# Kernel tuning notes

Hardware: AMD Instinct MI355X
Metric: run time of the kernel (lower is better)

## Reference

```python
import jax, jax.numpy as jnp
import numpy as np

ROUTING_ITERS = 3


def _squash(x, axis=-1):
    # sum_sq/(1+sum_sq) * x/sqrt(sum_sq), faithful to the torch squash
    sum_sq = jnp.sum(x * x, axis=axis, keepdims=True)
    return sum_sq / (1.0 + sum_sq) * x / jnp.sqrt(sum_sq)


def setup_inputs() -> dict:
    key = jax.random.key(0)
    k1, k2 = jax.random.split(key)
    B, I, O, Din, Dout = 256, 1152, 10, 8, 16
    x = jax.random.normal(k1, (B, I, Din), dtype=jnp.float32)
    W = jax.random.normal(k2, (I, O, Din, Dout), dtype=jnp.float32)
    return {"x": x, "W": W}


def reference(x, W):
    # x: [B, I, Din], W: [I, O, Din, Dout]
    I, O, Din, Dout = W.shape
    # u_hat = x @ W per (capsule_in, capsule_out): [B, I, O, Dout]
    u_hat = jnp.einsum('bid,iode->bioe', x, W)
    b = jnp.zeros((I, O), dtype=x.dtype)  # coupling logits, shared over batch
    v = None
    for _ in range(ROUTING_ITERS):
        c = jax.nn.softmax(b, axis=1)                    # softmax over out capsules
        s = jnp.einsum('bioe,io->boe', u_hat, c)         # weighted sum over in caps
        v = _squash(s, axis=-1)                          # [B, O, Dout]
        # agreement, averaged over batch (torch does .mean(dim=0))
        agree = jnp.einsum('bioe,boe->bio', u_hat, v).mean(axis=0)  # [I, O]
        b = b + agree
    # torch returns v.squeeze(1).transpose(2,3) -> [B, O, Dout, 1]
    return v[..., None]
```

## Files before the change

kernel.cpp:

```cpp
#include <hip/hip_runtime.h>
#include <math.h>

#define B    256
#define I    1152
#define O    10
#define DIN  8
#define DOUT 16
#define OE   160
#define XROW 9216
#define WROW 1280
#define PSPLIT 72
#define CHUNK  16
#define SI     8
#define GRID   288

#define WPREP_JOBS 720

typedef __attribute__((ext_vector_type(8))) short short8;
typedef __attribute__((ext_vector_type(4))) float floatx4;

#define AL(p)    __hip_atomic_load((p),      __ATOMIC_RELAXED, __HIP_MEMORY_SCOPE_AGENT)
#define AS(p, v) __hip_atomic_store((p), (v), __ATOMIC_RELAXED, __HIP_MEMORY_SCOPE_AGENT)

__device__ __forceinline__ unsigned short f2bf(float f) {
    unsigned u = __builtin_bit_cast(unsigned, f);
    u += 0x7fffu + ((u >> 16) & 1u);
    return (unsigned short)(u >> 16);
}
__device__ __forceinline__ float bf2f(unsigned short h) {
    unsigned u = ((unsigned)h) << 16;
    return __builtin_bit_cast(float, u);
}

__device__ __forceinline__ void gbar_full(unsigned* cnt, unsigned* gen)
{
    __syncthreads();
    if (threadIdx.x == 0) {
        __builtin_amdgcn_fence(__ATOMIC_RELEASE, "agent");
        unsigned g = __hip_atomic_load(gen, __ATOMIC_RELAXED, __HIP_MEMORY_SCOPE_AGENT);
        unsigned a = __hip_atomic_fetch_add(cnt, 1u, __ATOMIC_RELAXED, __HIP_MEMORY_SCOPE_AGENT);
        if (a == GRID - 1u) {
            __hip_atomic_store(cnt, 0u, __ATOMIC_RELAXED, __HIP_MEMORY_SCOPE_AGENT);
            __hip_atomic_store(gen, g + 1u, __ATOMIC_RELAXED, __HIP_MEMORY_SCOPE_AGENT);
        } else {
            unsigned spins = 0;
            while (__hip_atomic_load(gen, __ATOMIC_RELAXED, __HIP_MEMORY_SCOPE_AGENT) == g) {
                __builtin_amdgcn_s_sleep(4);
                if (++spins > (1u << 20)) break;
            }
        }
        __builtin_amdgcn_fence(__ATOMIC_ACQUIRE, "agent");
    }
    __syncthreads();
}

__device__ __forceinline__ void gbar_light(unsigned* cnt, unsigned* gen)
{
    __syncthreads();
    if (threadIdx.x == 0) {
        unsigned g = __hip_atomic_load(gen, __ATOMIC_RELAXED, __HIP_MEMORY_SCOPE_AGENT);
        unsigned a = __hip_atomic_fetch_add(cnt, 1u, __ATOMIC_RELAXED, __HIP_MEMORY_SCOPE_AGENT);
        if (a == GRID - 1u) {
            __hip_atomic_store(cnt, 0u, __ATOMIC_RELAXED, __HIP_MEMORY_SCOPE_AGENT);
            __hip_atomic_store(gen, g + 1u, __ATOMIC_RELEASE, __HIP_MEMORY_SCOPE_AGENT);
        } else {
            unsigned spins = 0;
            while (__hip_atomic_load(gen, __ATOMIC_RELAXED, __HIP_MEMORY_SCOPE_AGENT) == g) {
                __builtin_amdgcn_s_sleep(4);
                if (++spins > (1u << 20)) break;
            }
        }
    }
    __syncthreads();
}

__device__ __forceinline__ void stage_prep(
    int bid, int t,
    const float* __restrict__ x, const float* __restrict__ W,
    float* __restrict__ Wt,
    unsigned short* __restrict__ xTh, unsigned short* __restrict__ xTl,
    unsigned short* __restrict__ xh,  unsigned short* __restrict__ xl)
{
#pragma unroll
    for (int r = 0; r < 3; ++r) {
        int job = bid + GRID * r;
        if (job < WPREP_JOBS) {
            int g  = job * 256 + t;
            int i  = g / OE;
            int oe = g - i * OE;
            int o  = oe >> 4;
            int e  = oe & 15;
            const float* wp = W + (size_t)i * WROW + o * (DIN * DOUT) + e;
            float4 a, b;
            a.x = wp[0 * DOUT]; a.y = wp[1 * DOUT]; a.z = wp[2 * DOUT]; a.w = wp[3 * DOUT];
            b.x = wp[4 * DOUT]; b.y = wp[5 * DOUT]; b.z = wp[6 * DOUT]; b.w = wp[7 * DOUT];
            float4* dst = (float4*)(Wt + (size_t)g * 8);
            dst[0] = a;
            dst[1] = b;
        }
    }
#pragma unroll
    for (int r = 0; r < 4; ++r) {
        int g2  = bid + GRID * r;
        int idb = g2 % 144;
        int bb  = g2 / 144;
        int id  = idb * 64 + (t & 63);
        int b0  = bb * 32 + (t >> 6) * 8;
        float v[8];
#pragma unroll
        for (int j = 0; j < 8; ++j)
            v[j] = x[(size_t)(b0 + j) * XROW + id];
        short8 h8, l8;
#pragma unroll
        for (int j = 0; j < 8; ++j) {
            unsigned short h = f2bf(v[j]);
            h8[j] = (short)h;
            l8[j] = (short)f2bf(v[j] - bf2f(h));
        }
        *(short8*)(xTh + (size_t)id * B + b0) = h8;
        *(short8*)(xTl + (size_t)id * B + b0) = l8;
    }
#pragma unroll
    for (int r = 0; r < 8; ++r) {
        int g = (bid + GRID * r) * 256 + t;
        float4 v = ((const float4*)x)[g];
        ushort4 h, l;
        h.x = f2bf(v.x); l.x = f2bf(v.x - bf2f(h.x));
        h.y = f2bf(v.y); l.y = f2bf(v.y - bf2f(h.y));
        h.z = f2bf(v.z); l.z = f2bf(v.z - bf2f(h.z));
        h.w = f2bf(v.w); l.w = f2bf(v.w - bf2f(h.w));
        ((ushort4*)xh)[g] = h;
        ((ushort4*)xl)[g] = l;
    }
}

__device__ __forceinline__ void stage_spart(
    int bid, int t,
    unsigned short* __restrict__ Wh, unsigned short* __restrict__ Wl,
    float (*brow_s)[10], float (*cL)[10],
    const unsigned short* __restrict__ xh, const unsigned short* __restrict__ xl,
    const float* __restrict__ Wt,
    const float* __restrict__ a0, const float* __restrict__ a1,
    float* __restrict__ sp, int it)
{
    int ic  = bid >> 2;
    int mb  = (bid >> 1) & 1;
    int nb  = bid & 1;
    int b0  = mb * 128;
    int oe0 = nb * 80;
    int i0  = ic * CHUNK;

    int w    = t >> 6;
    int lane = t & 63;
    int l15  = lane & 15;
    int q    = lane >> 4;

    if (it) {
        if (t < 160) {
            int iL = t / 10;
            int o  = t - iL * 10;
            int i  = i0 + iL;
            float bo = AL(&a0[i * O + o]) * (1.f / (float)B);
            if (it == 2) bo += AL(&a1[i * O + o]) * (1.f / (float)B);
            brow_s[iL][o] = bo;
        }
        __syncthreads();
        if (t < 16) {
            float m = brow_s[t][0];
#pragma unroll
            for (int o = 1; o < O; ++o) m = fmaxf(m, brow_s[t][o]);
            float ex[O];
            float sum = 0.f;
#pragma unroll
            for (int o = 0; o < O; ++o) { ex[o] = __expf(brow_s[t][o] - m); sum += ex[o]; }
            float inv = 1.f / sum;
#pragma unroll
            for (int o = 0; o < O; ++o) cL[t][o] = ex[o] * inv;
        }
        __syncthreads();
    }

    floatx4 acc[2][5];
#pragma unroll
    for (int mt = 0; mt < 2; ++mt)
#pragma unroll
        for (int nt = 0; nt < 5; ++nt) acc[mt][nt] = (floatx4)(0.f);

#pragma unroll
    for (int round = 0; round < CHUNK / SI; ++round) {
        int si0 = i0 + round * SI;
        if (round) __syncthreads();

        short8 ah[2][2], al[2][2];
#pragma unroll
        for (int ks = 0; ks < 2; ++ks)
#pragma unroll
            for (int mt = 0; mt < 2; ++mt) {
                size_t goff = (size_t)(b0 + w * 32 + mt * 16 + l15) * XROW
                            + (size_t)si0 * 8 + (ks << 5) + (q << 3);
                ah[ks][mt] = *(const short8*)(xh + goff);
                al[ks][mt] = *(const short8*)(xl + goff);
            }

#pragma unroll
        for (int r = 0; r < 3; ++r) {
            int p = t + 256 * r;
            if (p < 640) {
                int oeL = p % 80;
                int iL  = p / 80;
                int o   = (oe0 + oeL) >> 4;
                const float* wp = Wt + ((size_t)(si0 + iL) * OE + oe0 + oeL) * 8;
                float cv = it ? cL[round * SI + iL][o] : 0.1f;
                float4 w0 = *(const float4*)wp;
                float4 w1 = *(const float4*)(wp + 4);
                float wv[8] = {w0.x, w0.y, w0.z, w0.w, w1.x, w1.y, w1.z, w1.w};
                short8 hv, lv;
#pragma unroll
                for (int d = 0; d < 8; ++d) {
                    float s = wv[d] * cv;
                    unsigned short h = f2bf(s);
                    hv[d] = (short)h;
                    lv[d] = (short)f2bf(s - bf2f(h));
                }
                int off = oeL * 64 + ((iL ^ (oeL & 7)) << 3);
                *(short8*)(Wh + off) = hv;
                *(short8*)(Wl + off) = lv;
            }
        }
        __syncthreads();

#pragma unroll
        for (int ks = 0; ks < 2; ++ks) {
#pragma unroll
            for (int nt = 0; nt < 5; ++nt) {
                int rn  = nt * 16 + l15;
                int off = rn * 64 + ((((ks << 2) + q) ^ (rn & 7)) << 3);
                short8 bh = *(const short8*)(Wh + off);
                short8 bl = *(const short8*)(Wl + off);
#pragma unroll
                for (int mt = 0; mt < 2; ++mt) {
                    acc[mt][nt] = __builtin_amdgcn_mfma_f32_16x16x32_bf16(ah[ks][mt], bh, acc[mt][nt], 0, 0, 0);
                    acc[mt][nt] = __builtin_amdgcn_mfma_f32_16x16x32_bf16(ah[ks][mt], bl, acc[mt][nt], 0, 0, 0);
                    acc[mt][nt] = __builtin_amdgcn_mfma_f32_16x16x32_bf16(al[ks][mt], bh, acc[mt][nt], 0, 0, 0);
                }
            }
        }
    }

    float* base = sp + (size_t)ic * (B * OE);
#pragma unroll
    for (int mt = 0; mt < 2; ++mt) {
        int row0 = b0 + w * 32 + mt * 16 + q * 4;
#pragma unroll
        for (int nt = 0; nt < 5; ++nt) {
            int col = oe0 + nt * 16 + l15;
#pragma unroll
            for (int reg = 0; reg < 4; ++reg)
                AS(&base[(row0 + reg) * OE + col], acc[mt][nt][reg]);
        }
    }
}

__device__ __forceinline__ void stage_vred(
    int bid, int t, const float* __restrict__ sp, float* __restrict__ out,
    unsigned* __restrict__ vT, int last)
{
    if (bid >= 160) return;
    int g = bid * 256 + t;
    float s = 0.f;
#pragma unroll 8
    for (int ic = 0; ic < PSPLIT; ++ic) s += AL(&sp[(size_t)ic * (B * OE) + g]);

    float ss = s * s;
    ss += __shfl_xor(ss, 1, 16);
    ss += __shfl_xor(ss, 2, 16);
    ss += __shfl_xor(ss, 4, 16);
    ss += __shfl_xor(ss, 8, 16);
    float f = sqrtf(ss) / (1.f + ss);
    float val = s * f;

    if (last) {
        out[g] = val;
    } else {
        int b  = g / OE;
        int oe = g - b * OE;
        unsigned short h = f2bf(val);
        unsigned pack = (unsigned)h | ((unsigned)f2bf(val - bf2f(h)) << 16);
        AS(&vT[oe * B + b], pack);
    }
}

__device__ __forceinline__ void stage_ggemm(
    int bid, int t,
    unsigned short* __restrict__ Vh, unsigned short* __restrict__ Vl,
    const unsigned short* __restrict__ xTh, const unsigned short* __restrict__ xTl,
    const unsigned* __restrict__ vT,
    const float* __restrict__ Wt, float* __restrict__ agree)
{
    if (bid >= 144) return;
    int m0  = (bid >> 1) * 128;
    int nb  = bid & 1;
    int oe0 = nb * 80;

    int w    = t >> 6;
    int lane = t & 63;
    int l15  = lane & 15;
    int q    = lane >> 4;

    floatx4 acc[2][5];
#pragma unroll
    for (int mt = 0; mt < 2; ++mt)
#pragma unroll
        for (int nt = 0; nt < 5; ++nt) acc[mt][nt] = (floatx4)(0.f);

#pragma unroll
    for (int win = 0; win < 4; ++win) {
        int k0 = win * 64;
        if (win) __syncthreads();

#pragma unroll
        for (int r = 0; r < 3; ++r) {
            int p = t + 256 * r;
            if (p < 640) {
                int row = p >> 3;
                int ch  = p & 7;
                const unsigned long long* vp =
                    (const unsigned long long*)(vT + (size_t)(oe0 + row) * B + k0 + (ch << 3));
                short8 hv, lv;
#pragma unroll
                for (int j = 0; j < 4; ++j) {
                    unsigned long long u = AL(&vp[j]);
                    unsigned lo = (unsigned)u, hi = (unsigned)(u >> 32);
                    hv[2 * j]     = (short)(lo & 0xffffu);
                    lv[2 * j]     = (short)(lo >> 16);
                    hv[2 * j + 1] = (short)(hi & 0xffffu);
                    lv[2 * j + 1] = (short)(hi >> 16);
                }
                int off = row * 64 + ((ch ^ (row & 7)) << 3);
                *(short8*)(Vh + off) = hv;
                *(short8*)(Vl + off) = lv;
            }
        }
        __syncthreads();

        short8 ah[2][2], al[2][2];
#pragma unroll
        for (int ks = 0; ks < 2; ++ks)
#pragma unroll
            for (int mt = 0; mt < 2; ++mt) {
                size_t ga = (size_t)(m0 + w * 32 + mt * 16 + l15) * B
                          + k0 + (ks << 5) + (q << 3);
                ah[ks][mt] = *(const short8*)(xTh + ga);
                al[ks][mt] = *(const short8*)(xTl + ga);
            }

#pragma unroll
        for (int ks = 0; ks < 2; ++ks) {
#pragma unroll
            for (int nt = 0; nt < 5; ++nt) {
                int rn  = nt * 16 + l15;
                int off = rn * 64 + ((((ks << 2) + q) ^ (rn & 7)) << 3);
                short8 bh = *(const short8*)(Vh + off);
                short8 bl = *(const short8*)(Vl + off);
#pragma unroll
                for (int mt = 0; mt < 2; ++mt) {
                    acc[mt][nt] = __builtin_amdgcn_mfma_f32_16x16x32_bf16(ah[ks][mt], bh, acc[mt][nt], 0, 0, 0);
                    acc[mt][nt] = __builtin_amdgcn_mfma_f32_16x16x32_bf16(ah[ks][mt], bl, acc[mt][nt], 0, 0, 0);
                    acc[mt][nt] = __builtin_amdgcn_mfma_f32_16x16x32_bf16(al[ks][mt], bh, acc[mt][nt], 0, 0, 0);
                }
            }
        }
    }

#pragma unroll
    for (int mt = 0; mt < 2; ++mt) {
        int rb = m0 + w * 32 + mt * 16 + q * 4;
        int i  = rb >> 3;
        int d0 = rb & 7;
#pragma unroll
        for (int nt = 0; nt < 5; ++nt) {
            int oe = oe0 + nt * 16 + l15;
            float4 wv = *(const float4*)(Wt + (size_t)i * WROW + oe * 8 + d0);
            floatx4 a = acc[mt][nt];
            float p = a[0] * wv.x + a[1] * wv.y + a[2] * wv.z + a[3] * wv.w;
            p += __shfl_xor(p, 1);
            p += __shfl_xor(p, 2);
            p += __shfl_xor(p, 4);
            p += __shfl_xor(p, 8);
            p += __shfl_xor(p, 16);
            if ((lane & 31) == 0)
                AS(&agree[i * O + nb * 5 + nt], p);
        }
    }
}

__global__ __launch_bounds__(256, 2) void mega_kernel(
    const float* __restrict__ x, const float* __restrict__ W,
    float* __restrict__ out, float* __restrict__ Wt,
    unsigned short* __restrict__ xTh, unsigned short* __restrict__ xTl,
    unsigned short* __restrict__ xh,  unsigned short* __restrict__ xl,
    unsigned* __restrict__ vT,
    float* __restrict__ sp, float* __restrict__ a0, float* __restrict__ a1,
    unsigned* __restrict__ bar)
{
    __shared__ unsigned short Sh[80 * 64], Sl[80 * 64];
    __shared__ float brow_s[16][10];
    __shared__ float cL[16][10];

    unsigned* cnt = bar;
    unsigned* gen = bar + 32;
    int bid = blockIdx.x;
    int t   = threadIdx.x;

    stage_prep(bid, t, x, W, Wt, xTh, xTl, xh, xl);
    gbar_full(cnt, gen);

    for (int it = 0; it < 3; ++it) {
        stage_spart(bid, t, Sh, Sl, brow_s, cL, xh, xl, Wt, a0, a1, sp, it);
        gbar_light(cnt, gen);
        stage_vred(bid, t, sp, out, vT, it == 2);
        if (it == 2) break;
        gbar_light(cnt, gen);
        stage_ggemm(bid, t, Sh, Sl, xTh, xTl, vT, Wt, it == 0 ? a0 : a1);
        gbar_light(cnt, gen);
    }
}

extern "C" void kernel_launch(void* const* d_in, const int* in_sizes, int n_in,
                              void* d_out, int out_size, void* d_ws, size_t ws_size,
                              hipStream_t stream)
{
    const float* x = (const float*)d_in[0];
    const float* W = (const float*)d_in[1];
    float* out = (float*)d_out;

    unsigned* bar = (unsigned*)d_ws;
    float* a0 = (float*)((char*)d_ws + 256);
    float* a1 = a0 + I * O;
    float* Wt = a1 + I * O;
    float* sp = Wt + (size_t)I * OE * DIN;
    unsigned short* xTh = (unsigned short*)(sp + (size_t)PSPLIT * B * OE);
    unsigned short* xTl = xTh + (size_t)XROW * B;
    unsigned short* xh  = xTl + (size_t)XROW * B;
    unsigned short* xl  = xh  + (size_t)XROW * B;
    unsigned* vT        = (unsigned*)(xl + (size_t)XROW * B);

    hipMemsetAsync(d_ws, 0, 256, stream);

    mega_kernel<<<GRID, 256, 0, stream>>>(
        x, W, out, Wt, xTh, xTl, xh, xl, vT, sp, a0, a1, bar);
}
```

Baseline: 176.1 us.

## Replace partial-sum buffer and reduction stage with atomic accumulation, fuse squash into agreement GEMM

Each block now atomically adds its partial s tile into a per-iteration zeroed buffer instead of writing 72 partial slices that a separate reduction stage sums. The squash and bf16 hi/lo split move into the agreement-GEMM staging, which removes the vT buffer and one grid barrier per routing iteration. The x fragments are also loaded into registers once before the routing loop. In exchange it adds float atomic contention on 40K addresses, makes the summation order nondeterministic, recomputes the squash redundantly across blocks, and raises register pressure.

```diff
diff --git a/kernel.cpp b/kernel.cpp
--- a/kernel.cpp
+++ b/kernel.cpp
@@ -79,7 +79,8 @@
     const float* __restrict__ x, const float* __restrict__ W,
     float* __restrict__ Wt,
     unsigned short* __restrict__ xTh, unsigned short* __restrict__ xTl,
-    unsigned short* __restrict__ xh,  unsigned short* __restrict__ xl)
+    unsigned short* __restrict__ xh,  unsigned short* __restrict__ xl,
+    float* __restrict__ sbase)
 {
 #pragma unroll
     for (int r = 0; r < 3; ++r) {
@@ -132,21 +133,26 @@
         ((ushort4*)xh)[g] = h;
         ((ushort4*)xl)[g] = l;
     }
+#pragma unroll
+    for (int r = 0; r < 2; ++r) {
+        int idx = (bid * 256 + t) + GRID * 256 * r;
+        if (idx < 3 * B * OE) AS(&sbase[idx], 0.f);
+    }
 }
 
 __device__ __forceinline__ void stage_spart(
     int bid, int t,
     unsigned short* __restrict__ Wh, unsigned short* __restrict__ Wl,
     float (*brow_s)[10], float (*cL)[10],
-    const unsigned short* __restrict__ xh, const unsigned short* __restrict__ xl,
+    const short8 (&xah)[2][2][2], const short8 (&xal)[2][2][2],
     const float* __restrict__ Wt,
     const float* __restrict__ a0, const float* __restrict__ a1,
-    float* __restrict__ sp, int it)
+    float* __restrict__ s_it, int it)
 {
     int ic  = bid >> 2;
-    int mb  = (bid >> 1) & 1;
     int nb  = bid & 1;
-    int b0  = mb * 128;
+    int mbq = (bid >> 1) & 1;
+    int b0  = mbq * 128;
     int oe0 = nb * 80;
     int i0  = ic * CHUNK;
 
@@ -160,8 +166,8 @@
             int iL = t / 10;
             int o  = t - iL * 10;
             int i  = i0 + iL;
-            float bo = AL(&a0[i * O + o]) * (1.f / (float)B);
-            if (it == 2) bo += AL(&a1[i * O + o]) * (1.f / (float)B);
+            float bo = a0[i * O + o] * (1.f / (float)B);
+            if (it == 2) bo += a1[i * O + o] * (1.f / (float)B);
             brow_s[iL][o] = bo;
         }
         __syncthreads();
@@ -190,17 +196,6 @@
     for (int round = 0; round < CHUNK / SI; ++round) {
         int si0 = i0 + round * SI;
         if (round) __syncthreads();
-
-        short8 ah[2][2], al[2][2];
-#pragma unroll
-        for (int ks = 0; ks < 2; ++ks)
-#pragma unroll
-            for (int mt = 0; mt < 2; ++mt) {
-                size_t goff = (size_t)(b0 + w * 32 + mt * 16 + l15) * XROW
-                            + (size_t)si0 * 8 + (ks << 5) + (q << 3);
-                ah[ks][mt] = *(const short8*)(xh + goff);
-                al[ks][mt] = *(const short8*)(xl + goff);
-            }
 
 #pragma unroll
         for (int r = 0; r < 3; ++r) {
@@ -239,15 +234,14 @@
                 short8 bl = *(const short8*)(Wl + off);
 #pragma unroll
                 for (int mt = 0; mt < 2; ++mt) {
-                    acc[mt][nt] = __builtin_amdgcn_mfma_f32_16x16x32_bf16(ah[ks][mt], bh, acc[mt][nt], 0, 0, 0);
-                    acc[mt][nt] = __builtin_amdgcn_mfma_f32_16x16x32_bf16(ah[ks][mt], bl, acc[mt][nt], 0, 0, 0);
-                    acc[mt][nt] = __builtin_amdgcn_mfma_f32_16x16x32_bf16(al[ks][mt], bh, acc[mt][nt], 0, 0, 0);
+                    acc[mt][nt] = __builtin_amdgcn_mfma_f32_16x16x32_bf16(xah[round][ks][mt], bh, acc[mt][nt], 0, 0, 0);
+                    acc[mt][nt] = __builtin_amdgcn_mfma_f32_16x16x32_bf16(xah[round][ks][mt], bl, acc[mt][nt], 0, 0, 0);
+                    acc[mt][nt] = __builtin_amdgcn_mfma_f32_16x16x32_bf16(xal[round][ks][mt], bh, acc[mt][nt], 0, 0, 0);
                 }
             }
         }
     }
 
-    float* base = sp + (size_t)ic * (B * OE);
 #pragma unroll
     for (int mt = 0; mt < 2; ++mt) {
         int row0 = b0 + w * 32 + mt * 16 + q * 4;
@@ -256,45 +250,16 @@
             int col = oe0 + nt * 16 + l15;
 #pragma unroll
             for (int reg = 0; reg < 4; ++reg)
-                AS(&base[(row0 + reg) * OE + col], acc[mt][nt][reg]);
-        }
-    }
-}
-
-__device__ __forceinline__ void stage_vred(
-    int bid, int t, const float* __restrict__ sp, float* __restrict__ out,
-    unsigned* __restrict__ vT, int last)
-{
-    if (bid >= 160) return;
-    int g = bid * 256 + t;
-    float s = 0.f;
-#pragma unroll 8
-    for (int ic = 0; ic < PSPLIT; ++ic) s += AL(&sp[(size_t)ic * (B * OE) + g]);
-
-    float ss = s * s;
-    ss += __shfl_xor(ss, 1, 16);
-    ss += __shfl_xor(ss, 2, 16);
-    ss += __shfl_xor(ss, 4, 16);
-    ss += __shfl_xor(ss, 8, 16);
-    float f = sqrtf(ss) / (1.f + ss);
-    float val = s * f;
-
-    if (last) {
-        out[g] = val;
-    } else {
-        int b  = g / OE;
-        int oe = g - b * OE;
-        unsigned short h = f2bf(val);
-        unsigned pack = (unsigned)h | ((unsigned)f2bf(val - bf2f(h)) << 16);
-        AS(&vT[oe * B + b], pack);
-    }
-}
-
-__device__ __forceinline__ void stage_ggemm(
+                atomicAdd(&s_it[(size_t)(row0 + reg) * OE + col], acc[mt][nt][reg]);
+        }
+    }
+}
+
+__device__ __forceinline__ void stage_ggemmv(
     int bid, int t,
     unsigned short* __restrict__ Vh, unsigned short* __restrict__ Vl,
     const unsigned short* __restrict__ xTh, const unsigned short* __restrict__ xTl,
-    const unsigned* __restrict__ vT,
+    const float* __restrict__ s_it,
     const float* __restrict__ Wt, float* __restrict__ agree)
 {
     if (bid >= 144) return;
@@ -319,27 +284,23 @@
         if (win) __syncthreads();
 
 #pragma unroll
-        for (int r = 0; r < 3; ++r) {
-            int p = t + 256 * r;
-            if (p < 640) {
-                int row = p >> 3;
-                int ch  = p & 7;
-                const unsigned long long* vp =
-                    (const unsigned long long*)(vT + (size_t)(oe0 + row) * B + k0 + (ch << 3));
-                short8 hv, lv;
-#pragma unroll
-                for (int j = 0; j < 4; ++j) {
-                    unsigned long long u = AL(&vp[j]);
-                    unsigned lo = (unsigned)u, hi = (unsigned)(u >> 32);
-                    hv[2 * j]     = (short)(lo & 0xffffu);
-                    lv[2 * j]     = (short)(lo >> 16);
-                    hv[2 * j + 1] = (short)(hi & 0xffffu);
-                    lv[2 * j + 1] = (short)(hi >> 16);
-                }
-                int off = row * 64 + ((ch ^ (row & 7)) << 3);
-                *(short8*)(Vh + off) = hv;
-                *(short8*)(Vl + off) = lv;
-            }
+        for (int r = 0; r < 20; ++r) {
+            int p   = t + 256 * r;
+            int bl  = p / 80;
+            int oeL = p - bl * 80;
+            float sv = s_it[(size_t)(k0 + bl) * OE + oe0 + oeL];
+            float ss = sv * sv;
+            ss += __shfl_xor(ss, 1, 16);
+            ss += __shfl_xor(ss, 2, 16);
+            ss += __shfl_xor(ss, 4, 16);
+            ss += __shfl_xor(ss, 8, 16);
+            float val = sv * (sqrtf(ss) / (1.f + ss));
+            unsigned short h = f2bf(val);
+            unsigned short lo = f2bf(val - bf2f(h));
+            int ch  = bl >> 3;
+            int off = oeL * 64 + ((ch ^ (oeL & 7)) << 3) + (bl & 7);
+            Vh[off] = h;
+            Vl[off] = lo;
         }
         __syncthreads();
 
@@ -394,13 +355,26 @@
     }
 }
 
+__device__ __forceinline__ void stage_out(
+    int bid, int t, const float* __restrict__ s_it, float* __restrict__ out)
+{
+    if (bid >= 160) return;
+    int g = bid * 256 + t;
+    float s = s_it[g];
+    float ss = s * s;
+    ss += __shfl_xor(ss, 1, 16);
+    ss += __shfl_xor(ss, 2, 16);
+    ss += __shfl_xor(ss, 4, 16);
+    ss += __shfl_xor(ss, 8, 16);
+    out[g] = s * (sqrtf(ss) / (1.f + ss));
+}
+
 __global__ __launch_bounds__(256, 2) void mega_kernel(
     const float* __restrict__ x, const float* __restrict__ W,
     float* __restrict__ out, float* __restrict__ Wt,
     unsigned short* __restrict__ xTh, unsigned short* __restrict__ xTl,
     unsigned short* __restrict__ xh,  unsigned short* __restrict__ xl,
-    unsigned* __restrict__ vT,
-    float* __restrict__ sp, float* __restrict__ a0, float* __restrict__ a1,
+    float* __restrict__ sbuf, float* __restrict__ a0, float* __restrict__ a1,
     unsigned* __restrict__ bar)
 {
     __shared__ unsigned short Sh[80 * 64], Sl[80 * 64];
@@ -412,17 +386,41 @@
     int bid = blockIdx.x;
     int t   = threadIdx.x;
 
-    stage_prep(bid, t, x, W, Wt, xTh, xTl, xh, xl);
+    if (t == 0) __builtin_amdgcn_fence(__ATOMIC_ACQUIRE, "agent");
+    __syncthreads();
+
+    stage_prep(bid, t, x, W, Wt, xTh, xTl, xh, xl, sbuf);
     gbar_full(cnt, gen);
 
+    short8 xah[2][2][2], xal[2][2][2];
+    {
+        int ic = bid >> 2;
+        int b0 = ((bid >> 1) & 1) * 128;
+        int i0 = ic * CHUNK;
+        int w = t >> 6, lane = t & 63, l15 = lane & 15, q = lane >> 4;
+#pragma unroll
+        for (int rd = 0; rd < 2; ++rd)
+#pragma unroll
+            for (int ks = 0; ks < 2; ++ks)
+#pragma unroll
+                for (int mt = 0; mt < 2; ++mt) {
+                    size_t goff = (size_t)(b0 + w * 32 + mt * 16 + l15) * XROW
+                                + (size_t)(i0 + rd * SI) * 8 + (ks << 5) + (q << 3);
+                    xah[rd][ks][mt] = *(const short8*)(xh + goff);
+                    xal[rd][ks][mt] = *(const short8*)(xl + goff);
+                }
+    }
+
     for (int it = 0; it < 3; ++it) {
-        stage_spart(bid, t, Sh, Sl, brow_s, cL, xh, xl, Wt, a0, a1, sp, it);
+        float* s_it = sbuf + (size_t)it * (B * OE);
+        stage_spart(bid, t, Sh, Sl, brow_s, cL, xah, xal, Wt, a0, a1, s_it, it);
         gbar_light(cnt, gen);
-        stage_vred(bid, t, sp, out, vT, it == 2);
-        if (it == 2) break;
-        gbar_light(cnt, gen);
-        stage_ggemm(bid, t, Sh, Sl, xTh, xTl, vT, Wt, it == 0 ? a0 : a1);
-        gbar_light(cnt, gen);
+        if (it < 2) {
+            stage_ggemmv(bid, t, Sh, Sl, xTh, xTl, s_it, Wt, it == 0 ? a0 : a1);
+            gbar_light(cnt, gen);
+        } else {
+            stage_out(bid, t, s_it, out);
+        }
     }
 }
 
@@ -435,18 +433,17 @@
     float* out = (float*)d_out;
 
     unsigned* bar = (unsigned*)d_ws;
-    float* a0 = (float*)((char*)d_ws + 256);
-    float* a1 = a0 + I * O;
-    float* Wt = a1 + I * O;
-    float* sp = Wt + (size_t)I * OE * DIN;
-    unsigned short* xTh = (unsigned short*)(sp + (size_t)PSPLIT * B * OE);
+    float* a0   = (float*)((char*)d_ws + 256);
+    float* a1   = a0 + I * O;
+    float* sbuf = a1 + I * O;
+    float* Wt   = sbuf + 3 * B * OE;
+    unsigned short* xTh = (unsigned short*)(Wt + (size_t)I * OE * DIN);
     unsigned short* xTl = xTh + (size_t)XROW * B;
     unsigned short* xh  = xTl + (size_t)XROW * B;
     unsigned short* xl  = xh  + (size_t)XROW * B;
-    unsigned* vT        = (unsigned*)(xl + (size_t)XROW * B);
 
     hipMemsetAsync(d_ws, 0, 256, stream);
 
     mega_kernel<<<GRID, 256, 0, stream>>>(
-        x, W, out, Wt, xTh, xTl, xh, xl, vT, sp, a0, a1, bar);
-}
+        x, W, out, Wt, xTh, xTl, xh, xl, sbuf, a0, a1, bar);
+}
```

New measurement: 311.8 us. +77.1%, slower.

## Halve s-partial split, vectorize reduction, and use per-iteration buffers instead of atomic loads

Applied to the files above, without the earlier changes.

Doubles the input-capsule chunk per spart block (PSPLIT 72→36), so only 144 blocks do the s-partial GEMM and the vred stage sums half as many partials. The reduction now uses float4 plain loads over 40 blocks. Per-iteration s-partial buffers and a second vT buffer replace relaxed atomic loads with ordinary loads, relying on the barriers' fences for visibility. The trade-off is less parallelism in the spart stage and stale-cache risk if the plain loads are not ordered by the barriers.

```diff
diff --git a/kernel.cpp b/kernel.cpp
--- a/kernel.cpp
+++ b/kernel.cpp
@@ -9,8 +9,8 @@
 #define OE   160
 #define XROW 9216
 #define WROW 1280
-#define PSPLIT 72
-#define CHUNK  16
+#define PSPLIT 36
+#define CHUNK  32
 #define SI     8
 #define GRID   288
 
@@ -19,7 +19,6 @@
 typedef __attribute__((ext_vector_type(8))) short short8;
 typedef __attribute__((ext_vector_type(4))) float floatx4;
 
-#define AL(p)    __hip_atomic_load((p),      __ATOMIC_RELAXED, __HIP_MEMORY_SCOPE_AGENT)
 #define AS(p, v) __hip_atomic_store((p), (v), __ATOMIC_RELAXED, __HIP_MEMORY_SCOPE_AGENT)
 
 __device__ __forceinline__ unsigned short f2bf(float f) {
@@ -141,12 +140,12 @@
     const unsigned short* __restrict__ xh, const unsigned short* __restrict__ xl,
     const float* __restrict__ Wt,
     const float* __restrict__ a0, const float* __restrict__ a1,
-    float* __restrict__ sp, int it)
+    float* __restrict__ sp_it, int it)
 {
     int ic  = bid >> 2;
-    int mb  = (bid >> 1) & 1;
     int nb  = bid & 1;
-    int b0  = mb * 128;
+    int mbq = (bid >> 1) & 1;
+    int b0  = mbq * 128;
     int oe0 = nb * 80;
     int i0  = ic * CHUNK;
 
@@ -156,16 +155,20 @@
     int q    = lane >> 4;
 
     if (it) {
-        if (t < 160) {
-            int iL = t / 10;
-            int o  = t - iL * 10;
-            int i  = i0 + iL;
-            float bo = AL(&a0[i * O + o]) * (1.f / (float)B);
-            if (it == 2) bo += AL(&a1[i * O + o]) * (1.f / (float)B);
-            brow_s[iL][o] = bo;
+#pragma unroll
+        for (int r = 0; r < 2; ++r) {
+            int p = t + 256 * r;
+            if (p < 320) {
+                int iL = p / 10;
+                int o  = p - iL * 10;
+                int i  = i0 + iL;
+                float bo = a0[i * O + o] * (1.f / (float)B);
+                if (it == 2) bo += a1[i * O + o] * (1.f / (float)B);
+                brow_s[iL][o] = bo;
+            }
         }
         __syncthreads();
-        if (t < 16) {
+        if (t < 32) {
             float m = brow_s[t][0];
 #pragma unroll
             for (int o = 1; o < O; ++o) m = fmaxf(m, brow_s[t][o]);
@@ -247,7 +250,7 @@
         }
     }
 
-    float* base = sp + (size_t)ic * (B * OE);
+    float* base = sp_it + (size_t)ic * (B * OE);
 #pragma unroll
     for (int mt = 0; mt < 2; ++mt) {
         int row0 = b0 + w * 32 + mt * 16 + q * 4;
@@ -262,31 +265,36 @@
 }
 
 __device__ __forceinline__ void stage_vred(
-    int bid, int t, const float* __restrict__ sp, float* __restrict__ out,
+    int bid, int t, const float* __restrict__ sp_it, float* __restrict__ out,
     unsigned* __restrict__ vT, int last)
 {
-    if (bid >= 160) return;
-    int g = bid * 256 + t;
-    float s = 0.f;
-#pragma unroll 8
-    for (int ic = 0; ic < PSPLIT; ++ic) s += AL(&sp[(size_t)ic * (B * OE) + g]);
-
-    float ss = s * s;
-    ss += __shfl_xor(ss, 1, 16);
-    ss += __shfl_xor(ss, 2, 16);
-    ss += __shfl_xor(ss, 4, 16);
-    ss += __shfl_xor(ss, 8, 16);
+    if (bid >= 40) return;
+    int qd = bid * 256 + t;
+    float4 s = {0.f, 0.f, 0.f, 0.f};
+#pragma unroll
+    for (int ic = 0; ic < PSPLIT; ++ic) {
+        float4 p = ((const float4*)(sp_it + (size_t)ic * (B * OE)))[qd];
+        s.x += p.x; s.y += p.y; s.z += p.z; s.w += p.w;
+    }
+    float ss = s.x * s.x + s.y * s.y + s.z * s.z + s.w * s.w;
+    ss += __shfl_xor(ss, 1);
+    ss += __shfl_xor(ss, 2);
     float f = sqrtf(ss) / (1.f + ss);
-    float val = s * f;
+    float4 val = {s.x * f, s.y * f, s.z * f, s.w * f};
 
     if (last) {
-        out[g] = val;
+        ((float4*)out)[qd] = val;
     } else {
-        int b  = g / OE;
-        int oe = g - b * OE;
-        unsigned short h = f2bf(val);
-        unsigned pack = (unsigned)h | ((unsigned)f2bf(val - bf2f(h)) << 16);
-        AS(&vT[oe * B + b], pack);
+        int e0 = qd * 4;
+        int b  = e0 / OE;
+        int oe = e0 - b * OE;
+        float vv[4] = {val.x, val.y, val.z, val.w};
+#pragma unroll
+        for (int j = 0; j < 4; ++j) {
+            unsigned short h = f2bf(vv[j]);
+            unsigned pack = (unsigned)h | ((unsigned)f2bf(vv[j] - bf2f(h)) << 16);
+            AS(&vT[(oe + j) * B + b], pack);
+        }
     }
 }
 
@@ -324,17 +332,15 @@
             if (p < 640) {
                 int row = p >> 3;
                 int ch  = p & 7;
-                const unsigned long long* vp =
-                    (const unsigned long long*)(vT + (size_t)(oe0 + row) * B + k0 + (ch << 3));
+                const unsigned* vp = vT + (size_t)(oe0 + row) * B + k0 + (ch << 3);
+                uint4 u0 = *(const uint4*)vp;
+                uint4 u1 = *(const uint4*)(vp + 4);
+                unsigned uu[8] = {u0.x, u0.y, u0.z, u0.w, u1.x, u1.y, u1.z, u1.w};
                 short8 hv, lv;
 #pragma unroll
-                for (int j = 0; j < 4; ++j) {
-                    unsigned long long u = AL(&vp[j]);
-                    unsigned lo = (unsigned)u, hi = (unsigned)(u >> 32);
-                    hv[2 * j]     = (short)(lo & 0xffffu);
-                    lv[2 * j]     = (short)(lo >> 16);
-                    hv[2 * j + 1] = (short)(hi & 0xffffu);
-                    lv[2 * j + 1] = (short)(hi >> 16);
+                for (int j = 0; j < 8; ++j) {
+                    hv[j] = (short)(uu[j] & 0xffffu);
+                    lv[j] = (short)(uu[j] >> 16);
                 }
                 int off = row * 64 + ((ch ^ (row & 7)) << 3);
                 *(short8*)(Vh + off) = hv;
@@ -399,26 +405,32 @@
     float* __restrict__ out, float* __restrict__ Wt,
     unsigned short* __restrict__ xTh, unsigned short* __restrict__ xTl,
     unsigned short* __restrict__ xh,  unsigned short* __restrict__ xl,
-    unsigned* __restrict__ vT,
-    float* __restrict__ sp, float* __restrict__ a0, float* __restrict__ a1,
+    unsigned* __restrict__ vT0, unsigned* __restrict__ vT1,
+    float* __restrict__ sbuf, float* __restrict__ a0, float* __restrict__ a1,
     unsigned* __restrict__ bar)
 {
     __shared__ unsigned short Sh[80 * 64], Sl[80 * 64];
-    __shared__ float brow_s[16][10];
-    __shared__ float cL[16][10];
+    __shared__ float brow_s[32][10];
+    __shared__ float cL[32][10];
 
     unsigned* cnt = bar;
     unsigned* gen = bar + 32;
     int bid = blockIdx.x;
     int t   = threadIdx.x;
 
+    if (t == 0) __builtin_amdgcn_fence(__ATOMIC_ACQUIRE, "agent");
+    __syncthreads();
+
     stage_prep(bid, t, x, W, Wt, xTh, xTl, xh, xl);
     gbar_full(cnt, gen);
 
     for (int it = 0; it < 3; ++it) {
-        stage_spart(bid, t, Sh, Sl, brow_s, cL, xh, xl, Wt, a0, a1, sp, it);
+        float* sp_it = sbuf + (size_t)it * PSPLIT * (B * OE);
+        unsigned* vT = (it == 0) ? vT0 : vT1;
+        if (bid < 4 * PSPLIT)
+            stage_spart(bid, t, Sh, Sl, brow_s, cL, xh, xl, Wt, a0, a1, sp_it, it);
         gbar_light(cnt, gen);
-        stage_vred(bid, t, sp, out, vT, it == 2);
+        stage_vred(bid, t, sp_it, out, vT, it == 2);
         if (it == 2) break;
         gbar_light(cnt, gen);
         stage_ggemm(bid, t, Sh, Sl, xTh, xTl, vT, Wt, it == 0 ? a0 : a1);
@@ -435,18 +447,19 @@
     float* out = (float*)d_out;
 
     unsigned* bar = (unsigned*)d_ws;
-    float* a0 = (float*)((char*)d_ws + 256);
-    float* a1 = a0 + I * O;
-    float* Wt = a1 + I * O;
-    float* sp = Wt + (size_t)I * OE * DIN;
-    unsigned short* xTh = (unsigned short*)(sp + (size_t)PSPLIT * B * OE);
+    float* a0   = (float*)((char*)d_ws + 256);
+    float* a1   = a0 + I * O;
+    float* Wt   = a1 + I * O;
+    float* sbuf = Wt + (size_t)I * OE * DIN;
+    unsigned short* xTh = (unsigned short*)(sbuf + (size_t)3 * PSPLIT * B * OE);
     unsigned short* xTl = xTh + (size_t)XROW * B;
     unsigned short* xh  = xTl + (size_t)XROW * B;
     unsigned short* xl  = xh  + (size_t)XROW * B;
-    unsigned* vT        = (unsigned*)(xl + (size_t)XROW * B);
+    unsigned* vT0       = (unsigned*)(xl + (size_t)XROW * B);
+    unsigned* vT1       = vT0 + B * OE;
 
     hipMemsetAsync(d_ws, 0, 256, stream);
 
     mega_kernel<<<GRID, 256, 0, stream>>>(
-        x, W, out, Wt, xTh, xTl, xh, xl, vT, sp, a0, a1, bar);
-}
+        x, W, out, Wt, xTh, xTl, xh, xl, vT0, vT1, sbuf, a0, a1, bar);
+}
```

New measurement: 203.9 us. 15.8% more time.
